# Kernel optimization log

Hardware: AMD Instinct MI355X
Metric: run time of the kernel (lower is better)

The kernel has to match this reference:

```python
import jax, jax.numpy as jnp
import numpy as np

PAD_ID = 12975
HEADS = 16


def _sinusoid_table(n_position, d_hid):
    # pos / 10000^(2*(j//2)/d_hid), sin on even dims, cos on odd dims
    pos = jnp.arange(n_position, dtype=jnp.float32)[:, None]          # [P,1]
    j = jnp.arange(d_hid)
    angle = pos / jnp.power(10000.0, (2.0 * (j // 2) / d_hid).astype(jnp.float32))  # [P,D]
    table = jnp.where((j % 2) == 0, jnp.sin(angle), jnp.cos(angle))
    return table  # [P, D]


def setup_inputs() -> dict:
    key = jax.random.key(0)
    k1, k2 = jax.random.split(key)
    x = jax.random.randint(k1, (256, 200), 0, 32000, dtype=jnp.int64)
    weight = jax.random.normal(k2, (32000, 1024), dtype=jnp.float32) * 0.02
    return {"x": x, "weight": weight}


def reference(x, weight):
    B, S = x.shape
    D = weight.shape[1]

    # --- mask build (faithful to the python-loop semantics) ---
    m = x == PAD_ID                                   # [B,S]
    has_pad = jnp.any(m, axis=1)                      # [B]
    first = jnp.argmax(m, axis=1)                     # first True index (0 if none)
    # torch loop: if no True found, i ends at S-1 and idx[S-1:] is still set True
    first = jnp.where(has_pad, first, S - 1)          # [B]
    row_ge = jnp.arange(S)[None, :] >= first[:, None]  # [B,S] rows >= first are all-True
    remask = m[:, None, :] | row_ge[:, :, None]       # [B,S,S]
    mask = jnp.broadcast_to(remask[:, None, :, :], (B, HEADS, S, S))  # [B,H,S,S]

    # --- embedding + sinusoidal positional encoding (dropout in eval = identity) ---
    emb = weight[x]                                   # [B,S,D]
    pos_table = _sinusoid_table(S, D)                 # [S,D]
    out = emb + pos_table[None, :, :]                 # [B,S,D]
    return (out, mask)
```

## Files before the change

### kernel.cpp

```cpp
#include <hip/hip_runtime.h>
#include <math.h>

#define PAD_ID 12975
#define BB 256
#define SS 200
#define DD 1024
#define HH 16

#define MASK_CHUNKS (BB * HH * SS * (SS / 4))
#define OUT_ROWS    (BB * SS)

#define NBLK 2048
#define MBLK 1376

typedef float f32x4 __attribute__((ext_vector_type(4)));
typedef int   i32x4 __attribute__((ext_vector_type(4)));

#define WS_FIRST_BYTES 1024
#define WS_POST_BYTES  (SS * DD * 4)

__global__ void prep_kernel(const int* __restrict__ x, int* __restrict__ first,
                            float* __restrict__ posT) {
    const int idx = blockIdx.x * blockDim.x + threadIdx.x;
    if (idx < SS * DD) {
        const int s = idx >> 10;
        const int j = idx & (DD - 1);
        const int p = j >> 1;
        const float C = (float)(13.287712379549449 / 512.0);
        const float angle = (float)s / exp2f((float)p * C);
        posT[idx] = (j & 1) ? cosf(angle) : sinf(angle);
    }
    if (blockIdx.x < BB) {
        __shared__ int sfirst;
        if (threadIdx.x == 0) sfirst = SS - 1;
        __syncthreads();
        if (threadIdx.x < SS && x[blockIdx.x * SS + threadIdx.x] == PAD_ID)
            atomicMin(&sfirst, threadIdx.x);
        __syncthreads();
        if (threadIdx.x == 0) first[blockIdx.x] = sfirst;
    }
}

__global__ void work_kernel(const int* __restrict__ x, const int* __restrict__ first,
                            const float* __restrict__ weight, const float* __restrict__ posT,
                            float* __restrict__ out, float* __restrict__ mask) {
    if (blockIdx.x < MBLK) {
        const int stride = MBLK * 256;
        for (int c = blockIdx.x * 256 + threadIdx.x; c < MASK_CHUNKS; c += stride) {
            const int row = c / 50;
            const int j4  = c - row * 50;
            const int b   = row / (HH * SS);
            const int i   = row % SS;
            f32x4 v;
            if (i >= first[b]) {
                v = (f32x4){1.f, 1.f, 1.f, 1.f};
            } else {
                const i32x4 xv = ((const i32x4*)x)[b * 50 + j4];
                v.x = (xv.x == PAD_ID) ? 1.f : 0.f;
                v.y = (xv.y == PAD_ID) ? 1.f : 0.f;
                v.z = (xv.z == PAD_ID) ? 1.f : 0.f;
                v.w = (xv.w == PAD_ID) ? 1.f : 0.f;
            }
            __builtin_nontemporal_store(v, (f32x4*)mask + c);
        }
    } else {
        const int ob = blockIdx.x - MBLK;
        const int OB = NBLK - MBLK;
        for (int row = ob; row < OUT_ROWS; row += OB) {
            const int s   = row % SS;
            const int idx = x[row];
            const int t   = threadIdx.x;
            const f32x4 w  = ((const f32x4*)(weight + (size_t)idx * DD))[t];
            const f32x4 pe = ((const f32x4*)(posT + (size_t)s * DD))[t];
            const f32x4 r = w + pe;
            __builtin_nontemporal_store(r, (f32x4*)(out + (size_t)row * DD) + t);
        }
    }
}

extern "C" void kernel_launch(void* const* d_in, const int* in_sizes, int n_in,
                              void* d_out, int out_size, void* d_ws, size_t ws_size,
                              hipStream_t stream) {
    const int*   x      = (const int*)d_in[0];
    const float* weight = (const float*)d_in[1];
    float* out  = (float*)d_out;
    float* mask = out + (size_t)BB * SS * DD;

    int*   first = (int*)d_ws;
    float* posT  = (float*)((char*)d_ws + WS_FIRST_BYTES);

    prep_kernel<<<(SS * DD + 255) / 256, 256, 0, stream>>>(x, first, posT);
    work_kernel<<<NBLK, 256, 0, stream>>>(x, first, weight, posT, out, mask);
}
```

Before: 161.0 us.

## Fuse prep into work kernel and compute positional encoding inline

Removes the separate prep kernel launch. Each mask block now computes the first-pad index for all batches into shared memory, and the embedding blocks compute sin/cos positional encoding in registers instead of reading a precomputed table. This drops one launch and the table write/read traffic. In exchange it adds redundant first-pad scans in every mask block and transcendental math per element, and it rebalances the block split between mask and embedding work. Inline angle uses s*exp2(-k) vs s/exp2(k), slight numeric difference.

```diff
diff --git a/kernel.cpp b/kernel.cpp
--- a/kernel.cpp
+++ b/kernel.cpp
@@ -11,40 +11,31 @@
 #define OUT_ROWS    (BB * SS)
 
 #define NBLK 2048
-#define MBLK 1376
+#define MBLK 1280
 
 typedef float f32x4 __attribute__((ext_vector_type(4)));
 typedef int   i32x4 __attribute__((ext_vector_type(4)));
 
-#define WS_FIRST_BYTES 1024
-#define WS_POST_BYTES  (SS * DD * 4)
-
-__global__ void prep_kernel(const int* __restrict__ x, int* __restrict__ first,
-                            float* __restrict__ posT) {
-    const int idx = blockIdx.x * blockDim.x + threadIdx.x;
-    if (idx < SS * DD) {
-        const int s = idx >> 10;
-        const int j = idx & (DD - 1);
-        const int p = j >> 1;
-        const float C = (float)(13.287712379549449 / 512.0);
-        const float angle = (float)s / exp2f((float)p * C);
-        posT[idx] = (j & 1) ? cosf(angle) : sinf(angle);
-    }
-    if (blockIdx.x < BB) {
-        __shared__ int sfirst;
-        if (threadIdx.x == 0) sfirst = SS - 1;
-        __syncthreads();
-        if (threadIdx.x < SS && x[blockIdx.x * SS + threadIdx.x] == PAD_ID)
-            atomicMin(&sfirst, threadIdx.x);
-        __syncthreads();
-        if (threadIdx.x == 0) first[blockIdx.x] = sfirst;
-    }
-}
-
-__global__ void work_kernel(const int* __restrict__ x, const int* __restrict__ first,
-                            const float* __restrict__ weight, const float* __restrict__ posT,
+__global__ void work_kernel(const int* __restrict__ x, const float* __restrict__ weight,
                             float* __restrict__ out, float* __restrict__ mask) {
     if (blockIdx.x < MBLK) {
+        __shared__ int sfirst[BB];
+        {
+            const int t = threadIdx.x;
+            int f = SS - 1;
+            const i32x4* xr = (const i32x4*)(x + t * SS);
+            #pragma unroll 10
+            for (int j4 = 49; j4 >= 0; --j4) {
+                const i32x4 v = xr[j4];
+                const int base = j4 * 4;
+                if (v.w == PAD_ID) f = base + 3 < f ? base + 3 : f;
+                if (v.z == PAD_ID) f = base + 2 < f ? base + 2 : f;
+                if (v.y == PAD_ID) f = base + 1 < f ? base + 1 : f;
+                if (v.x == PAD_ID) f = base + 0 < f ? base + 0 : f;
+            }
+            sfirst[t] = f;
+        }
+        __syncthreads();
         const int stride = MBLK * 256;
         for (int c = blockIdx.x * 256 + threadIdx.x; c < MASK_CHUNKS; c += stride) {
             const int row = c / 50;
@@ -52,7 +43,7 @@
             const int b   = row / (HH * SS);
             const int i   = row % SS;
             f32x4 v;
-            if (i >= first[b]) {
+            if (i >= sfirst[b]) {
                 v = (f32x4){1.f, 1.f, 1.f, 1.f};
             } else {
                 const i32x4 xv = ((const i32x4*)x)[b * 50 + j4];
@@ -64,16 +55,21 @@
             __builtin_nontemporal_store(v, (f32x4*)mask + c);
         }
     } else {
+        const int t = threadIdx.x;
+        const float C = (float)(13.287712379549449 / 512.0);
+        const float rd0 = exp2f(-(float)(2 * t) * C);
+        const float rd1 = exp2f(-(float)(2 * t + 1) * C);
         const int ob = blockIdx.x - MBLK;
         const int OB = NBLK - MBLK;
         for (int row = ob; row < OUT_ROWS; row += OB) {
             const int s   = row % SS;
             const int idx = x[row];
-            const int t   = threadIdx.x;
-            const f32x4 w  = ((const f32x4*)(weight + (size_t)idx * DD))[t];
-            const f32x4 pe = ((const f32x4*)(posT + (size_t)s * DD))[t];
-            const f32x4 r = w + pe;
-            __builtin_nontemporal_store(r, (f32x4*)(out + (size_t)row * DD) + t);
+            const float fs = (float)s;
+            const float a0 = fs * rd0;
+            const float a1 = fs * rd1;
+            const f32x4 pe = (f32x4){sinf(a0), cosf(a0), sinf(a1), cosf(a1)};
+            const f32x4 w = ((const f32x4*)(weight + (size_t)idx * DD))[t];
+            __builtin_nontemporal_store(w + pe, (f32x4*)(out + (size_t)row * DD) + t);
         }
     }
 }
@@ -86,9 +82,5 @@
     float* out  = (float*)d_out;
     float* mask = out + (size_t)BB * SS * DD;
 
-    int*   first = (int*)d_ws;
-    float* posT  = (float*)((char*)d_ws + WS_FIRST_BYTES);
-
-    prep_kernel<<<(SS * DD + 255) / 256, 256, 0, stream>>>(x, first, posT);
-    work_kernel<<<NBLK, 256, 0, stream>>>(x, first, weight, posT, out, mask);
+    work_kernel<<<NBLK, 256, 0, stream>>>(x, weight, out, mask);
 }
```

Result: slower. 172.4 us (+7.1%).
